# Kernel tuning notes

Measured on AMD Instinct MI355X. Metric: run time of the kernel, lower is better.

The kernel has to match this reference:

```python
import jax, jax.numpy as jnp
import numpy as np


def gcn_conv(x, src, dst, W, b, N):
    """PyG GCNConv: add self-loops, symmetric D^-1/2 (A+I) D^-1/2 normalization."""
    loop = jnp.arange(N, dtype=src.dtype)
    s = jnp.concatenate([src, loop])
    d = jnp.concatenate([dst, loop])
    deg = jnp.zeros((N,), dtype=x.dtype).at[d].add(1.0)  # in-degree incl. self-loop
    dinv = jax.lax.rsqrt(deg)  # deg >= 1 because of self-loops
    norm = dinv[s] * dinv[d]  # [E+N]
    h = x @ W  # [N, out] linear transform first (as in PyG)
    msg = h[s] * norm[:, None]  # gather + scale
    out = jax.ops.segment_sum(msg, d, num_segments=N)  # scatter-add
    return out + b


def setup_inputs() -> dict:
    key = jax.random.key(0)
    ks = jax.random.split(key, 10)
    N, E, in_dim, h1, h2, A = 100000, 3200000, 256, 32, 64, 64
    x = jax.random.normal(ks[0], (N, in_dim), dtype=jnp.float32)
    ei = jax.random.randint(ks[1], (2, E), 0, N, dtype=jnp.int64)
    def glorot(k, shape):
        lim = float(np.sqrt(6.0 / (shape[0] + shape[1])))
        return jax.random.uniform(k, shape, jnp.float32, -lim, lim)
    return {
        "x": x,
        "ei": ei,
        "num_nodes": N,
        "W1": glorot(ks[2], (in_dim, h1)), "b1": jnp.zeros((h1,), jnp.float32),
        "W2": glorot(ks[3], (h1, h2)),     "b2": jnp.zeros((h2,), jnp.float32),
        "Wo1": glorot(ks[4], (h2, h2)),    "bo1": jnp.zeros((h2,), jnp.float32),
        "Wo2": glorot(ks[5], (h2, A)),     "bo2": jnp.zeros((A,), jnp.float32),
    }


def reference(x, ei, num_nodes, W1, b1, W2, b2, Wo1, bo1, Wo2, bo2):
    src, dst = ei[0], ei[1]
    z = jax.nn.relu(gcn_conv(x, src, dst, W1, b1, num_nodes))
    z = jax.nn.relu(gcn_conv(z, src, dst, W2, b2, num_nodes))
    logits = jax.nn.relu(z @ Wo1 + bo1) @ Wo2 + bo2  # [N, action_space]
    nbatches = z.shape[0] // num_nodes
    # original reshapes with z.size(1)=hidden2 (== action_space here)
    dist = logits.reshape(nbatches, num_nodes * z.shape[1])
    return jax.nn.softmax(dist, axis=-1)  # Categorical probs
```

## Files before the change

### kernel.cpp

```cpp
#include <hip/hip_runtime.h>

#define DEVI __device__ __forceinline__

DEVI unsigned fkey(float f) {
  unsigned u = __float_as_uint(f);
  return u ^ ((u >> 31) ? 0xFFFFFFFFu : 0x80000000u);
}
DEVI float funkey(unsigned k) {
  unsigned b = (k & 0x80000000u) ? (k ^ 0x80000000u) : ~k;
  return __uint_as_float(b);
}
DEVI float f4get(const float4& v, int j) {
  return j == 0 ? v.x : j == 1 ? v.y : j == 2 ? v.z : v.w;
}

constexpr int BSH = 9;
constexpr int BNODES = 1 << BSH;
constexpr int PEPT = 16;
constexpr int PCHUNK = 256 * PEPT;

__global__ void k_binit(int* __restrict__ bcnt) {
  bcnt[threadIdx.x] = 0;
}

__global__ void k_bcount(const int* __restrict__ dst, int* __restrict__ bcnt,
                         int E, int NB) {
  __shared__ int lh[256];
  lh[threadIdx.x] = 0;
  __syncthreads();
  int stride = gridDim.x * 256;
  for (long i = (long)blockIdx.x * 256 + threadIdx.x; i < E; i += stride)
    atomicAdd(&lh[dst[i] >> BSH], 1);
  __syncthreads();
  if (threadIdx.x < NB && lh[threadIdx.x]) atomicAdd(&bcnt[threadIdx.x], lh[threadIdx.x]);
}

__global__ void k_bscan(const int* __restrict__ bcnt, int* __restrict__ bbase,
                        int* __restrict__ bcur, unsigned* __restrict__ scal, int NB) {
  __shared__ int s[256];
  int t = threadIdx.x;
  int v = (t < NB) ? bcnt[t] : 0;
  s[t] = v;
  __syncthreads();
  for (int o = 1; o < 256; o <<= 1) {
    int add = (t >= o) ? s[t - o] : 0;
    __syncthreads();
    s[t] += add;
    __syncthreads();
  }
  int excl = s[t] - v;
  if (t < NB) { bbase[t] = excl; bcur[t] = excl; }
  if (t == 0) { scal[0] = 0u; scal[1] = 0u; }
}

__global__ __launch_bounds__(256)
void k_bpart(const int* __restrict__ src, const int* __restrict__ dst,
             int* __restrict__ bcur, unsigned* __restrict__ epart, int E, int NB) {
  __shared__ int lh[256];
  __shared__ int gbase[256];
  long base = (long)blockIdx.x * PCHUNK;
  lh[threadIdx.x] = 0;
  __syncthreads();
  int ed[PEPT]; int es[PEPT]; unsigned short lpos[PEPT];
#pragma unroll
  for (int j = 0; j < PEPT; j++) {
    long i = base + threadIdx.x + (long)j * 256;
    if (i < E) {
      int d = dst[i];
      es[j] = src[i];
      ed[j] = d;
      lpos[j] = (unsigned short)atomicAdd(&lh[d >> BSH], 1);
    } else {
      ed[j] = -1;
    }
  }
  __syncthreads();
  if (threadIdx.x < NB) {
    int c = lh[threadIdx.x];
    gbase[threadIdx.x] = c ? atomicAdd(&bcur[threadIdx.x], c) : 0;
  }
  __syncthreads();
#pragma unroll
  for (int j = 0; j < PEPT; j++) {
    int d = ed[j];
    if (d >= 0) {
      unsigned p = (unsigned)(gbase[d >> BSH] + (int)lpos[j]);
      epart[p] = ((unsigned)(d & (BNODES - 1)) << 17) | (unsigned)es[j];
    }
  }
}

__global__ __launch_bounds__(256)
void k_fine(const unsigned* __restrict__ epart, const int* __restrict__ bbase,
            const int* __restrict__ bcnt, int* __restrict__ rowptr,
            int* __restrict__ deg, float* __restrict__ dinv,
            int* __restrict__ col, int N) {
  __shared__ int lh[BNODES];
  __shared__ int lexcl[BNODES];
  __shared__ int ssc[256];
  int b = blockIdx.x;
  int base = bbase[b], cnt = bcnt[b];
  int nlo = b << BSH;
  int t = threadIdx.x;
  lh[t] = 0; lh[t + 256] = 0;
  __syncthreads();
  for (int i = t; i < cnt; i += 256) {
    unsigned e = epart[base + i];
    atomicAdd(&lh[e >> 17], 1);
  }
  __syncthreads();
  int a0 = lh[2 * t], a1 = lh[2 * t + 1];
  ssc[t] = a0 + a1;
  __syncthreads();
  for (int o = 1; o < 256; o <<= 1) {
    int add = (t >= o) ? ssc[t - o] : 0;
    __syncthreads();
    ssc[t] += add;
    __syncthreads();
  }
  int excl = ssc[t] - (a0 + a1);
  lexcl[2 * t] = excl;
  lexcl[2 * t + 1] = excl + a0;
  __syncthreads();
#pragma unroll
  for (int k = 0; k < 2; k++) {
    int i = t + k * 256;
    int v = nlo + i;
    if (v < N) {
      int dgv = lh[i];
      deg[v] = dgv;
      rowptr[v] = base + lexcl[i];
      dinv[v] = rsqrtf((float)(dgv + 1));
    }
  }
  __syncthreads();
  lh[2 * t] = lexcl[2 * t];
  lh[2 * t + 1] = lexcl[2 * t + 1];
  __syncthreads();
  for (int i = t; i < cnt; i += 256) {
    unsigned e = epart[base + i];
    int p = atomicAdd(&lh[e >> 17], 1);
    col[base + p] = (int)(e & 0x1FFFFu);
  }
}

__global__ __launch_bounds__(256)
void k_gemm1(const float* __restrict__ in, const float* __restrict__ W,
             const float* __restrict__ dinv, float* __restrict__ out, int N) {
  __shared__ float Wl[256 * 32];
  __shared__ float xb[2][128 * 16];
  const int t = threadIdx.x;

  {
    const float4* W4 = (const float4*)W;
    float4* Wl4 = (float4*)Wl;
#pragma unroll
    for (int i = 0; i < 8; i++) Wl4[t + i * 256] = W4[t + i * 256];
  }

  const int srow = t >> 1;
  const int part = t & 1;
  const int sk = (srow >> 1) & 3;
  long grow = (long)blockIdx.x * 128 + srow;
  const float* gsrc = in + (grow < (long)N ? grow : (long)(N - 1)) * 256 + part * 8;
  const int q0 = part * 2, q1 = part * 2 + 1;
  const int ws0 = srow * 16 + ((q0 ^ sk) << 2);
  const int ws1 = srow * 16 + ((q1 ^ sk) << 2);

  const int cg = t & 3;
  const int rg = t >> 2;
  const int c0 = cg * 8;
  const int rk = (rg >> 1) & 3;

  {
    float4 a = *(const float4*)(gsrc + 0);
    float4 b = *(const float4*)(gsrc + 4);
    *(float4*)&xb[0][ws0] = a;
    *(float4*)&xb[0][ws1] = b;
  }
  __syncthreads();

  float acc[2][8];
#pragma unroll
  for (int i = 0; i < 2; i++)
#pragma unroll
    for (int c = 0; c < 8; c++) acc[i][c] = 0.f;

  for (int ch = 0; ch < 16; ch++) {
    float4 na, nb;
    if (ch < 15) {
      na = *(const float4*)(gsrc + (ch + 1) * 16 + 0);
      nb = *(const float4*)(gsrc + (ch + 1) * 16 + 4);
    }
    const float* xc = xb[ch & 1];
#pragma unroll
    for (int q = 0; q < 4; q++) {
      float4 xv0 = *(const float4*)&xc[rg * 16 + ((q ^ rk) << 2)];
      float4 xv1 = *(const float4*)&xc[(rg + 64) * 16 + ((q ^ rk) << 2)];
#pragma unroll
      for (int jj = 0; jj < 4; jj++) {
        const float* wr = &Wl[(ch * 16 + q * 4 + jj) * 32 + c0];
        float4 wa = *(const float4*)(wr);
        float4 wb = *(const float4*)(wr + 4);
        float x0 = f4get(xv0, jj);
        float x1 = f4get(xv1, jj);
        acc[0][0] = fmaf(x0, wa.x, acc[0][0]);
        acc[0][1] = fmaf(x0, wa.y, acc[0][1]);
        acc[0][2] = fmaf(x0, wa.z, acc[0][2]);
        acc[0][3] = fmaf(x0, wa.w, acc[0][3]);
        acc[0][4] = fmaf(x0, wb.x, acc[0][4]);
        acc[0][5] = fmaf(x0, wb.y, acc[0][5]);
        acc[0][6] = fmaf(x0, wb.z, acc[0][6]);
        acc[0][7] = fmaf(x0, wb.w, acc[0][7]);
        acc[1][0] = fmaf(x1, wa.x, acc[1][0]);
        acc[1][1] = fmaf(x1, wa.y, acc[1][1]);
        acc[1][2] = fmaf(x1, wa.z, acc[1][2]);
        acc[1][3] = fmaf(x1, wa.w, acc[1][3]);
        acc[1][4] = fmaf(x1, wb.x, acc[1][4]);
        acc[1][5] = fmaf(x1, wb.y, acc[1][5]);
        acc[1][6] = fmaf(x1, wb.z, acc[1][6]);
        acc[1][7] = fmaf(x1, wb.w, acc[1][7]);
      }
    }
    if (ch < 15) {
      __syncthreads();
      float* xn = xb[(ch + 1) & 1];
      *(float4*)&xn[ws0] = na;
      *(float4*)&xn[ws1] = nb;
      __syncthreads();
    }
  }

#pragma unroll
  for (int i = 0; i < 2; i++) {
    long r = (long)blockIdx.x * 128 + rg + i * 64;
    if (r < (long)N) {
      float dv = dinv[r];
      float* op = &out[r * 32 + c0];
      *(float4*)(op) = make_float4(acc[i][0] * dv, acc[i][1] * dv,
                                   acc[i][2] * dv, acc[i][3] * dv);
      *(float4*)(op + 4) = make_float4(acc[i][4] * dv, acc[i][5] * dv,
                                       acc[i][6] * dv, acc[i][7] * dv);
    }
  }
}

template <int K, int COLS, int ROWS, bool BIAS, bool RELU, bool SCALE, bool DOMAX>
__launch_bounds__(256)
__global__ void k_gemm(const float* __restrict__ in, const float* __restrict__ W,
                       const float* __restrict__ bias, const float* __restrict__ dinv,
                       float* __restrict__ out, int N, unsigned* __restrict__ gmax) {
  constexpr int CG = COLS / 8;
  constexpr int RG = 256 / CG;
  constexpr int RPB = RG * ROWS;
  __shared__ float Wl[K * COLS];
  for (int i = threadIdx.x; i < K * COLS; i += 256) Wl[i] = W[i];
  __syncthreads();

  int cg = threadIdx.x % CG, rg = threadIdx.x / CG;
  int c0 = cg * 8;
  long r0 = (long)blockIdx.x * RPB + rg * ROWS;

  float acc[ROWS][8];
#pragma unroll
  for (int i = 0; i < ROWS; i++)
#pragma unroll
    for (int c = 0; c < 8; c++) acc[i][c] = 0.f;
  bool rv[ROWS];
#pragma unroll
  for (int i = 0; i < ROWS; i++) rv[i] = (r0 + i) < (long)N;

  const float* ip = in + r0 * K;
#pragma unroll 2
  for (int k = 0; k < K; k += 4) {
    float4 xv[ROWS];
#pragma unroll
    for (int i = 0; i < ROWS; i++)
      xv[i] = rv[i] ? *(const float4*)(ip + (long)i * K + k) : make_float4(0.f, 0.f, 0.f, 0.f);
#pragma unroll
    for (int jj = 0; jj < 4; jj++) {
      const float4 wa = *(const float4*)&Wl[(k + jj) * COLS + c0];
      const float4 wb = *(const float4*)&Wl[(k + jj) * COLS + c0 + 4];
#pragma unroll
      for (int i = 0; i < ROWS; i++) {
        float xs = f4get(xv[i], jj);
        acc[i][0] = fmaf(xs, wa.x, acc[i][0]);
        acc[i][1] = fmaf(xs, wa.y, acc[i][1]);
        acc[i][2] = fmaf(xs, wa.z, acc[i][2]);
        acc[i][3] = fmaf(xs, wa.w, acc[i][3]);
        acc[i][4] = fmaf(xs, wb.x, acc[i][4]);
        acc[i][5] = fmaf(xs, wb.y, acc[i][5]);
        acc[i][6] = fmaf(xs, wb.z, acc[i][6]);
        acc[i][7] = fmaf(xs, wb.w, acc[i][7]);
      }
    }
  }

  float bo[8];
  if (BIAS) {
#pragma unroll
    for (int c = 0; c < 8; c++) bo[c] = bias[c0 + c];
  }
  float m = -3.4e38f;
#pragma unroll
  for (int i = 0; i < ROWS; i++) {
    if (!rv[i]) continue;
    float dv = SCALE ? dinv[r0 + i] : 1.f;
    float o[8];
#pragma unroll
    for (int c = 0; c < 8; c++) {
      float v = acc[i][c];
      if (BIAS) v += bo[c];
      if (SCALE) v *= dv;
      if (RELU) v = fmaxf(v, 0.f);
      if (DOMAX) m = fmaxf(m, v);
      o[c] = v;
    }
    float* op = &out[(r0 + i) * COLS + c0];
    *(float4*)(op) = make_float4(o[0], o[1], o[2], o[3]);
    *(float4*)(op + 4) = make_float4(o[4], o[5], o[6], o[7]);
  }
  if constexpr (DOMAX) {
    __shared__ float red[256];
    red[threadIdx.x] = m;
    __syncthreads();
    for (int o = 128; o > 0; o >>= 1) {
      if (threadIdx.x < o) red[threadIdx.x] = fmaxf(red[threadIdx.x], red[threadIdx.x + o]);
      __syncthreads();
    }
    if (threadIdx.x == 0) atomicMax(gmax, fkey(red[0]));
  }
}

template <int FEAT, bool BIAS, bool RELU, bool PSCALE>
__launch_bounds__(256)
__global__ void k_aggv(const float* __restrict__ g, const int* __restrict__ col,
                       const int* __restrict__ rowptr, const int* __restrict__ deg,
                       const float* __restrict__ dinv, const float* __restrict__ bias,
                       float* __restrict__ out, int N) {
  constexpr int LPN = FEAT / 4;
  constexpr int NPB = 256 / LPN;
  int nib = threadIdx.x / LPN;
  int c = threadIdx.x % LPN;
  long v = (long)blockIdx.x * NPB + nib;
  if (v >= N) return;

  const float4* g4 = (const float4*)g;
  float4 acc = g4[v * LPN + c];
  int start = rowptr[v], dg = deg[v];
  int e = 0;
  while (e < dg) {
    int cnt = min(LPN, dg - e);
    int idx = (c < cnt) ? col[start + e + c] : 0;
    int j = 0;
    for (; j + 4 <= cnt; j += 4) {
      int u0 = __shfl(idx, j + 0, LPN);
      int u1 = __shfl(idx, j + 1, LPN);
      int u2 = __shfl(idx, j + 2, LPN);
      int u3 = __shfl(idx, j + 3, LPN);
      float4 a0 = g4[(long)u0 * LPN + c];
      float4 a1 = g4[(long)u1 * LPN + c];
      float4 a2 = g4[(long)u2 * LPN + c];
      float4 a3 = g4[(long)u3 * LPN + c];
      acc.x += (a0.x + a1.x) + (a2.x + a3.x);
      acc.y += (a0.y + a1.y) + (a2.y + a3.y);
      acc.z += (a0.z + a1.z) + (a2.z + a3.z);
      acc.w += (a0.w + a1.w) + (a2.w + a3.w);
    }
    for (; j < cnt; j++) {
      int u = __shfl(idx, j, LPN);
      float4 a = g4[(long)u * LPN + c];
      acc.x += a.x; acc.y += a.y; acc.z += a.z; acc.w += a.w;
    }
    e += cnt;
  }
  float dv = dinv[v];
  float4 val;
  val.x = acc.x * dv; val.y = acc.y * dv; val.z = acc.z * dv; val.w = acc.w * dv;
  if (BIAS) {
    float4 b = ((const float4*)bias)[c];
    val.x += b.x; val.y += b.y; val.z += b.z; val.w += b.w;
  }
  if (RELU) {
    val.x = fmaxf(val.x, 0.f); val.y = fmaxf(val.y, 0.f);
    val.z = fmaxf(val.z, 0.f); val.w = fmaxf(val.w, 0.f);
  }
  if (PSCALE) {
    val.x *= dv; val.y *= dv; val.z *= dv; val.w *= dv;
  }
  ((float4*)out)[v * LPN + c] = val;
}

__global__ void k_smsum(const float* __restrict__ logit, unsigned* __restrict__ scal, int total) {
  __shared__ float s[256];
  float gmax = funkey(scal[0]);
  float loc = 0.f;
  for (int i = blockIdx.x * 256 + threadIdx.x; i < total; i += gridDim.x * 256)
    loc += expf(logit[i] - gmax);
  s[threadIdx.x] = loc; __syncthreads();
  for (int o = 128; o > 0; o >>= 1) {
    if (threadIdx.x < o) s[threadIdx.x] += s[threadIdx.x + o];
    __syncthreads();
  }
  if (threadIdx.x == 0) atomicAdd((float*)&scal[1], s[0]);
}

__global__ void k_smnorm(float* __restrict__ logit, const unsigned* __restrict__ scal, int total) {
  float gmax = funkey(scal[0]);
  float inv = 1.0f / __uint_as_float(scal[1]);
  int i = blockIdx.x * 256 + threadIdx.x;
  if (i < total) logit[i] = expf(logit[i] - gmax) * inv;
}

extern "C" void kernel_launch(void* const* d_in, const int* in_sizes, int n_in,
                              void* d_out, int out_size, void* d_ws, size_t ws_size,
                              hipStream_t stream) {
  const float* x   = (const float*)d_in[0];
  const int*   ei  = (const int*)d_in[1];
  const float* W1  = (const float*)d_in[3];
  const float* b1  = (const float*)d_in[4];
  const float* W2  = (const float*)d_in[5];
  const float* b2  = (const float*)d_in[6];
  const float* Wo1 = (const float*)d_in[7];
  const float* bo1 = (const float*)d_in[8];
  const float* Wo2 = (const float*)d_in[9];
  const float* bo2 = (const float*)d_in[10];

  const int N = in_sizes[0] / 256;
  const int E = in_sizes[1] / 2;
  const int* src = ei;
  const int* dst = ei + E;
  const int NB = (N + BNODES - 1) / BNODES;

  size_t o = 0;
  auto carve = [&](size_t bytes) -> char* {
    char* p = (char*)d_ws + o;
    o += (bytes + 255) & ~(size_t)255;
    return p;
  };
  float* R1     = (float*)carve((size_t)N * 64 * 4);
  float* R2     = (float*)carve((size_t)N * 64 * 4);
  int*   col    = (int*)carve((size_t)E * 4);
  int*   deg    = (int*)carve((size_t)N * 4);
  float* dinv   = (float*)carve((size_t)N * 4);
  int*   rowptr = (int*)carve((size_t)N * 4);
  int*   bcnt   = (int*)carve(256 * 4);
  int*   bbase  = (int*)carve(256 * 4);
  int*   bcur   = (int*)carve(256 * 4);
  unsigned* scal = (unsigned*)carve(64);

  unsigned* epart = (unsigned*)R2;
  float* g1 = R1;
  float* p  = R2;
  float* s2 = R1;
  float* z2 = R2;
  float* t  = R1;
  float* logits = (float*)d_out;

  k_binit<<<1, 256, 0, stream>>>(bcnt);
  k_bcount<<<512, 256, 0, stream>>>(dst, bcnt, E, NB);
  k_bscan<<<1, 256, 0, stream>>>(bcnt, bbase, bcur, scal, NB);
  k_bpart<<<(E + PCHUNK - 1) / PCHUNK, 256, 0, stream>>>(src, dst, bcur, epart, E, NB);
  k_fine<<<NB, 256, 0, stream>>>(epart, bbase, bcnt, rowptr, deg, dinv, col, N);

  const int g1G = (N + 127) / 128;
  const int gG = (N + 63) / 64;
  const int gA = (N + 31) / 32;

  k_gemm1<<<g1G, 256, 0, stream>>>(x, W1, dinv, g1, N);
  k_aggv<32, true, true, true><<<gA, 256, 0, stream>>>(g1, col, rowptr, deg, dinv, b1, p, N);

  k_aggv<32, false, false, false><<<gA, 256, 0, stream>>>(p, col, rowptr, deg, dinv, nullptr, s2, N);
  k_gemm<32, 64, 2, true, true, false, false>
      <<<gG, 256, 0, stream>>>(s2, W2, b2, nullptr, z2, N, nullptr);

  k_gemm<64, 64, 2, true, true, false, false>
      <<<gG, 256, 0, stream>>>(z2, Wo1, bo1, nullptr, t, N, nullptr);
  k_gemm<64, 64, 2, true, false, false, true>
      <<<gG, 256, 0, stream>>>(t, Wo2, bo2, nullptr, logits, N, scal);

  k_smsum<<<1024, 256, 0, stream>>>(logits, scal, out_size);
  k_smnorm<<<(out_size + 255) / 256, 256, 0, stream>>>(logits, scal, out_size);
}
```

Baseline: 517.6 us.

## Fuse three head GEMMs into one kernel keeping intermediates in shared memory

Replaces the three separate dense-layer kernels (W2, Wo1, Wo2) with a single kernel that processes 128 rows per block. Intermediate activations stay in a swizzled shared-memory buffer instead of round-tripping through global memory, and the weights are staged once per block. This removes two full N×64 write/read passes and two launches. In exchange it uses about 64KB of LDS per block, which may reduce occupancy.

```diff
diff --git a/kernel.cpp b/kernel.cpp
--- a/kernel.cpp
+++ b/kernel.cpp
@@ -245,44 +245,118 @@
   }
 }
 
-template <int K, int COLS, int ROWS, bool BIAS, bool RELU, bool SCALE, bool DOMAX>
-__launch_bounds__(256)
-__global__ void k_gemm(const float* __restrict__ in, const float* __restrict__ W,
-                       const float* __restrict__ bias, const float* __restrict__ dinv,
-                       float* __restrict__ out, int N, unsigned* __restrict__ gmax) {
-  constexpr int CG = COLS / 8;
-  constexpr int RG = 256 / CG;
-  constexpr int RPB = RG * ROWS;
-  __shared__ float Wl[K * COLS];
-  for (int i = threadIdx.x; i < K * COLS; i += 256) Wl[i] = W[i];
-  __syncthreads();
-
-  int cg = threadIdx.x % CG, rg = threadIdx.x / CG;
-  int c0 = cg * 8;
-  long r0 = (long)blockIdx.x * RPB + rg * ROWS;
-
-  float acc[ROWS][8];
-#pragma unroll
-  for (int i = 0; i < ROWS; i++)
+__global__ __launch_bounds__(256)
+void k_head(const float* __restrict__ s2,
+            const float* __restrict__ W2, const float* __restrict__ b2,
+            const float* __restrict__ Wo1, const float* __restrict__ bo1,
+            const float* __restrict__ Wo2, const float* __restrict__ bo2,
+            float* __restrict__ out, int N, unsigned* __restrict__ gmax) {
+  __shared__ float A[64 * 64];
+  __shared__ float B[64 * 64];
+  __shared__ float xr[128 * 64];
+  const int t = threadIdx.x;
+  const int cg = t & 7, rg = t >> 3;
+  const int c0 = cg * 8;
+  const int key = rg & 7;
+  const long r0 = (long)blockIdx.x * 128 + rg * 4;
+
+  {
+    const float4* w2 = (const float4*)W2;
+    const float4* w1 = (const float4*)Wo1;
+    float4* Af = (float4*)A;
+    float4* Bf = (float4*)B;
+    Af[t] = w2[t];
+    Af[t + 256] = w2[t + 256];
+#pragma unroll
+    for (int i = 0; i < 4; i++) Bf[t + i * 256] = w1[t + i * 256];
+  }
+  __syncthreads();
+
+  bool rv[4];
+  int xrow[4];
+#pragma unroll
+  for (int i = 0; i < 4; i++) {
+    rv[i] = (r0 + i) < (long)N;
+    xrow[i] = (rg + 32 * i) * 64;
+  }
+
+  float acc[4][8];
+
+#pragma unroll
+  for (int i = 0; i < 4; i++)
 #pragma unroll
     for (int c = 0; c < 8; c++) acc[i][c] = 0.f;
-  bool rv[ROWS];
-#pragma unroll
-  for (int i = 0; i < ROWS; i++) rv[i] = (r0 + i) < (long)N;
-
-  const float* ip = in + r0 * K;
+  {
+    const float* ip = s2 + r0 * 32;
 #pragma unroll 2
-  for (int k = 0; k < K; k += 4) {
-    float4 xv[ROWS];
-#pragma unroll
-    for (int i = 0; i < ROWS; i++)
-      xv[i] = rv[i] ? *(const float4*)(ip + (long)i * K + k) : make_float4(0.f, 0.f, 0.f, 0.f);
+    for (int k = 0; k < 32; k += 4) {
+      float4 xv[4];
+#pragma unroll
+      for (int i = 0; i < 4; i++)
+        xv[i] = rv[i] ? *(const float4*)(ip + i * 32 + k)
+                      : make_float4(0.f, 0.f, 0.f, 0.f);
+#pragma unroll
+      for (int jj = 0; jj < 4; jj++) {
+        float4 wa = *(const float4*)&A[(k + jj) * 64 + c0];
+        float4 wb = *(const float4*)&A[(k + jj) * 64 + c0 + 4];
+#pragma unroll
+        for (int i = 0; i < 4; i++) {
+          float xs = f4get(xv[i], jj);
+          acc[i][0] = fmaf(xs, wa.x, acc[i][0]);
+          acc[i][1] = fmaf(xs, wa.y, acc[i][1]);
+          acc[i][2] = fmaf(xs, wa.z, acc[i][2]);
+          acc[i][3] = fmaf(xs, wa.w, acc[i][3]);
+          acc[i][4] = fmaf(xs, wb.x, acc[i][4]);
+          acc[i][5] = fmaf(xs, wb.y, acc[i][5]);
+          acc[i][6] = fmaf(xs, wb.z, acc[i][6]);
+          acc[i][7] = fmaf(xs, wb.w, acc[i][7]);
+        }
+      }
+    }
+    float bo[8];
+#pragma unroll
+    for (int c = 0; c < 8; c++) bo[c] = b2[c0 + c];
+    const int q0 = (2 * cg) ^ key, q1 = (2 * cg + 1) ^ key;
+#pragma unroll
+    for (int i = 0; i < 4; i++) {
+      float v0 = fmaxf(acc[i][0] + bo[0], 0.f);
+      float v1 = fmaxf(acc[i][1] + bo[1], 0.f);
+      float v2 = fmaxf(acc[i][2] + bo[2], 0.f);
+      float v3 = fmaxf(acc[i][3] + bo[3], 0.f);
+      float v4 = fmaxf(acc[i][4] + bo[4], 0.f);
+      float v5 = fmaxf(acc[i][5] + bo[5], 0.f);
+      float v6 = fmaxf(acc[i][6] + bo[6], 0.f);
+      float v7 = fmaxf(acc[i][7] + bo[7], 0.f);
+      *(float4*)&xr[xrow[i] + 4 * q0] = make_float4(v0, v1, v2, v3);
+      *(float4*)&xr[xrow[i] + 4 * q1] = make_float4(v4, v5, v6, v7);
+    }
+  }
+  __syncthreads();
+
+  float4 wo2r[4];
+  {
+    const float4* w = (const float4*)Wo2;
+#pragma unroll
+    for (int i = 0; i < 4; i++) wo2r[i] = w[t + i * 256];
+  }
+
+#pragma unroll
+  for (int i = 0; i < 4; i++)
+#pragma unroll
+    for (int c = 0; c < 8; c++) acc[i][c] = 0.f;
+#pragma unroll 2
+  for (int k = 0; k < 64; k += 4) {
+    const int q = k >> 2;
+    float4 xv[4];
+#pragma unroll
+    for (int i = 0; i < 4; i++)
+      xv[i] = *(const float4*)&xr[xrow[i] + 4 * (q ^ key)];
 #pragma unroll
     for (int jj = 0; jj < 4; jj++) {
-      const float4 wa = *(const float4*)&Wl[(k + jj) * COLS + c0];
-      const float4 wb = *(const float4*)&Wl[(k + jj) * COLS + c0 + 4];
-#pragma unroll
-      for (int i = 0; i < ROWS; i++) {
+      float4 wa = *(const float4*)&B[(k + jj) * 64 + c0];
+      float4 wb = *(const float4*)&B[(k + jj) * 64 + c0 + 4];
+#pragma unroll
+      for (int i = 0; i < 4; i++) {
         float xs = f4get(xv[i], jj);
         acc[i][0] = fmaf(xs, wa.x, acc[i][0]);
         acc[i][1] = fmaf(xs, wa.y, acc[i][1]);
@@ -295,41 +369,89 @@
       }
     }
   }
-
-  float bo[8];
-  if (BIAS) {
-#pragma unroll
-    for (int c = 0; c < 8; c++) bo[c] = bias[c0 + c];
+  __syncthreads();
+
+  {
+    float4* Af = (float4*)A;
+#pragma unroll
+    for (int i = 0; i < 4; i++) Af[t + i * 256] = wo2r[i];
+    float bo[8];
+#pragma unroll
+    for (int c = 0; c < 8; c++) bo[c] = bo1[c0 + c];
+    const int q0 = (2 * cg) ^ key, q1 = (2 * cg + 1) ^ key;
+#pragma unroll
+    for (int i = 0; i < 4; i++) {
+      float v0 = fmaxf(acc[i][0] + bo[0], 0.f);
+      float v1 = fmaxf(acc[i][1] + bo[1], 0.f);
+      float v2 = fmaxf(acc[i][2] + bo[2], 0.f);
+      float v3 = fmaxf(acc[i][3] + bo[3], 0.f);
+      float v4 = fmaxf(acc[i][4] + bo[4], 0.f);
+      float v5 = fmaxf(acc[i][5] + bo[5], 0.f);
+      float v6 = fmaxf(acc[i][6] + bo[6], 0.f);
+      float v7 = fmaxf(acc[i][7] + bo[7], 0.f);
+      *(float4*)&xr[xrow[i] + 4 * q0] = make_float4(v0, v1, v2, v3);
+      *(float4*)&xr[xrow[i] + 4 * q1] = make_float4(v4, v5, v6, v7);
+    }
+  }
+  __syncthreads();
+
+#pragma unroll
+  for (int i = 0; i < 4; i++)
+#pragma unroll
+    for (int c = 0; c < 8; c++) acc[i][c] = 0.f;
+#pragma unroll 2
+  for (int k = 0; k < 64; k += 4) {
+    const int q = k >> 2;
+    float4 xv[4];
+#pragma unroll
+    for (int i = 0; i < 4; i++)
+      xv[i] = *(const float4*)&xr[xrow[i] + 4 * (q ^ key)];
+#pragma unroll
+    for (int jj = 0; jj < 4; jj++) {
+      float4 wa = *(const float4*)&A[(k + jj) * 64 + c0];
+      float4 wb = *(const float4*)&A[(k + jj) * 64 + c0 + 4];
+#pragma unroll
+      for (int i = 0; i < 4; i++) {
+        float xs = f4get(xv[i], jj);
+        acc[i][0] = fmaf(xs, wa.x, acc[i][0]);
+        acc[i][1] = fmaf(xs, wa.y, acc[i][1]);
+        acc[i][2] = fmaf(xs, wa.z, acc[i][2]);
+        acc[i][3] = fmaf(xs, wa.w, acc[i][3]);
+        acc[i][4] = fmaf(xs, wb.x, acc[i][4]);
+        acc[i][5] = fmaf(xs, wb.y, acc[i][5]);
+        acc[i][6] = fmaf(xs, wb.z, acc[i][6]);
+        acc[i][7] = fmaf(xs, wb.w, acc[i][7]);
+      }
+    }
   }
   float m = -3.4e38f;
-#pragma unroll
-  for (int i = 0; i < ROWS; i++) {
-    if (!rv[i]) continue;
-    float dv = SCALE ? dinv[r0 + i] : 1.f;
-    float o[8];
-#pragma unroll
-    for (int c = 0; c < 8; c++) {
-      float v = acc[i][c];
-      if (BIAS) v += bo[c];
-      if (SCALE) v *= dv;
-      if (RELU) v = fmaxf(v, 0.f);
-      if (DOMAX) m = fmaxf(m, v);
-      o[c] = v;
-    }
-    float* op = &out[(r0 + i) * COLS + c0];
-    *(float4*)(op) = make_float4(o[0], o[1], o[2], o[3]);
-    *(float4*)(op + 4) = make_float4(o[4], o[5], o[6], o[7]);
-  }
-  if constexpr (DOMAX) {
-    __shared__ float red[256];
-    red[threadIdx.x] = m;
+  {
+    float bo[8];
+#pragma unroll
+    for (int c = 0; c < 8; c++) bo[c] = bo2[c0 + c];
+#pragma unroll
+    for (int i = 0; i < 4; i++) {
+      if (!rv[i]) continue;
+      float o[8];
+#pragma unroll
+      for (int c = 0; c < 8; c++) {
+        float v = acc[i][c] + bo[c];
+        m = fmaxf(m, v);
+        o[c] = v;
+      }
+      float* op = &out[(r0 + i) * 64 + c0];
+      *(float4*)(op) = make_float4(o[0], o[1], o[2], o[3]);
+      *(float4*)(op + 4) = make_float4(o[4], o[5], o[6], o[7]);
+    }
+  }
+  __syncthreads();
+  xr[t] = m;
+  __syncthreads();
+  for (int o2 = 128; o2 > 0; o2 >>= 1) {
+    if (t < o2) xr[t] = fmaxf(xr[t], xr[t + o2]);
     __syncthreads();
-    for (int o = 128; o > 0; o >>= 1) {
-      if (threadIdx.x < o) red[threadIdx.x] = fmaxf(red[threadIdx.x], red[threadIdx.x + o]);
-      __syncthreads();
-    }
-    if (threadIdx.x == 0) atomicMax(gmax, fkey(red[0]));
-  }
+  }
+  if (t == 0) atomicMax(gmax, fkey(xr[0]));
 }
 
 template <int FEAT, bool BIAS, bool RELU, bool PSCALE>
@@ -453,8 +575,6 @@
   float* g1 = R1;
   float* p  = R2;
   float* s2 = R1;
-  float* z2 = R2;
-  float* t  = R1;
   float* logits = (float*)d_out;
 
   k_binit<<<1, 256, 0, stream>>>(bcnt);
@@ -464,20 +584,14 @@
   k_fine<<<NB, 256, 0, stream>>>(epart, bbase, bcnt, rowptr, deg, dinv, col, N);
 
   const int g1G = (N + 127) / 128;
-  const int gG = (N + 63) / 64;
   const int gA = (N + 31) / 32;
 
   k_gemm1<<<g1G, 256, 0, stream>>>(x, W1, dinv, g1, N);
   k_aggv<32, true, true, true><<<gA, 256, 0, stream>>>(g1, col, rowptr, deg, dinv, b1, p, N);
 
   k_aggv<32, false, false, false><<<gA, 256, 0, stream>>>(p, col, rowptr, deg, dinv, nullptr, s2, N);
-  k_gemm<32, 64, 2, true, true, false, false>
-      <<<gG, 256, 0, stream>>>(s2, W2, b2, nullptr, z2, N, nullptr);
-
-  k_gemm<64, 64, 2, true, true, false, false>
-      <<<gG, 256, 0, stream>>>(z2, Wo1, bo1, nullptr, t, N, nullptr);
-  k_gemm<64, 64, 2, true, false, false, true>
-      <<<gG, 256, 0, stream>>>(t, Wo2, bo2, nullptr, logits, N, scal);
+
+  k_head<<<g1G, 256, 0, stream>>>(s2, W2, b2, Wo1, bo1, Wo2, bo2, logits, N, scal);
 
   k_smsum<<<1024, 256, 0, stream>>>(logits, scal, out_size);
   k_smnorm<<<(out_size + 255) / 256, 256, 0, stream>>>(logits, scal, out_size);
```

Result: faster. 495.9 us (-4.2%).
